# Kernel tuning notes

Measured on AMD Instinct MI355X. Metric: run time of the kernel, lower is better.

## Reference

```python
import jax, jax.numpy as jnp
import numpy as np

B, N, C = 2, 4096, 1024
H, WIN = 16, 20
D = C // H

def setup_inputs() -> dict:
    key = jax.random.key(0)
    ks = jax.random.split(key, 9)
    s = 1.0 / np.sqrt(C)
    d = {"q": jax.random.normal(ks[0], (B, N, C), jnp.float32)}
    for i, name in enumerate(["Wq", "Wk", "Wv", "Wo"]):
        d[name + "_w"] = jax.random.normal(ks[1 + 2 * i], (C, C), jnp.float32) * s
        d[name + "_b"] = jax.random.normal(ks[2 + 2 * i], (C,), jnp.float32) * 0.01
    return d

def reference(q, Wq_w, Wq_b, Wk_w, Wk_b, Wv_w, Wv_b, Wo_w, Wo_b):
    b, n, c = q.shape
    w2 = WIN // 2  # half window = 10
    def proj(x, w, bias):
        return (x @ w.T + bias).reshape(b, n, H, D).transpose(0, 2, 1, 3)  # [B,H,N,D]
    Q = proj(q, Wq_w, Wq_b)
    K = proj(q, Wk_w, Wk_b)
    V = proj(q, Wv_w, Wv_b)
    off = jnp.arange(-w2, w2 + 1)                       # [Wn] = 21 offsets
    pos = jnp.arange(n)[:, None] + off[None, :]         # [N, Wn] key index per query
    valid = (pos >= 0) & (pos < n)                      # edge clipping == torch start/end slicing
    idx = jnp.clip(pos, 0, n - 1)
    Kw = K[:, :, idx, :]                                # [B,H,N,Wn,D] gathered key windows
    Vw = V[:, :, idx, :]
    scale = jnp.sqrt(jnp.float32(D))
    scores = jnp.einsum('bhnd,bhnwd->bhnw', Q, Kw) / scale
    scores = jnp.where(valid[None, None], scores, -jnp.inf)
    probs = jax.nn.softmax(scores, axis=-1)             # invalid slots get exactly 0
    out = jnp.einsum('bhnw,bhnwd->bhnd', probs, Vw)
    out = out.transpose(0, 2, 1, 3).reshape(b, n, c)
    out = out @ Wo_w.T + Wo_b
    # torch returns attn_probs of the LAST loop iteration i=N-1: window [N-1-w2, N), size w2+1
    attn_last = probs[:, :, -1:, : w2 + 1]              # [B,H,1,11]
    return (out, attn_last)
```

## Files before the change

kernel.cpp:

```cpp
#include <hip/hip_runtime.h>
#include <hip/hip_bf16.h>

#define Bb 2
#define Nn 4096
#define Cc 1024
#define Hh 16
#define Dd 64
#define Mm (Bb*Nn)
#define W2 10
#define WINSZ 21

typedef __attribute__((ext_vector_type(8))) short  bf16x8s;
typedef __attribute__((ext_vector_type(4))) float  f32x4;
typedef __attribute__((ext_vector_type(4))) unsigned short us4;

#define AS1 __attribute__((address_space(1)))
#define AS3 __attribute__((address_space(3)))

__device__ __forceinline__ unsigned short f2bf(float f) {
  unsigned int u = __float_as_uint(f);
  u += 0x7FFFu + ((u >> 16) & 1u);
  return (unsigned short)(u >> 16);
}
__device__ __forceinline__ float bflo(unsigned int u) { return __uint_as_float(u << 16); }
__device__ __forceinline__ float bfhi(unsigned int u) { return __uint_as_float(u & 0xFFFF0000u); }

__global__ __launch_bounds__(256) void f2bf_kernel(const float4* __restrict__ src,
                                                   us4* __restrict__ dst, int n4) {
  int stride = gridDim.x * 256;
  for (int i = blockIdx.x * 256 + threadIdx.x; i < n4; i += stride) {
    float4 v = src[i];
    us4 o;
    o.x = f2bf(v.x); o.y = f2bf(v.y); o.z = f2bf(v.z); o.w = f2bf(v.w);
    dst[i] = o;
  }
}

template<bool OUT_BF16>
__global__ __launch_bounds__(512) void gemm_p3(const unsigned short* __restrict__ A,
                                               const unsigned short* __restrict__ Bm,
                                               const float* __restrict__ bias,
                                               void* __restrict__ Cout,
                                               int N) {
  constexpr int K = 1024, NT = 16;
  __shared__ unsigned short lds[3][24576];

  const int tid = threadIdx.x, wid = tid >> 6, lane = tid & 63;
  const int wm = wid >> 2, wn = wid & 3;

  const int nwg = gridDim.x, cpx = nwg >> 3, bid = blockIdx.x;
  const int swz = (bid & 7) * cpx + (bid >> 3);
  const int nbn = N >> 8;
  const int m0 = (swz / nbn) << 7, n0 = (swz % nbn) << 8;

  const int rbase = wid * 8 + (lane >> 3);
  const int cst = ((lane & 7) ^ (lane >> 3)) * 8;
  const unsigned short* aS0 = A + (size_t)(m0 + rbase) * K + cst;
  const unsigned short* aS1 = A + (size_t)(m0 + 64 + rbase) * K + cst;
  const unsigned short* bS0 = Bm + (size_t)(n0 + rbase) * K + cst;
  const unsigned short* bS1 = Bm + (size_t)(n0 + 64 + rbase) * K + cst;
  const unsigned short* bS2 = Bm + (size_t)(n0 + 128 + rbase) * K + cst;
  const unsigned short* bS3 = Bm + (size_t)(n0 + 192 + rbase) * K + cst;
  const int dA0 = wid * 512, dA1 = 4096 + wid * 512;
  const int dB0 = 8192 + wid * 512, dB1 = 12288 + wid * 512;
  const int dB2 = 16384 + wid * 512, dB3 = 20480 + wid * 512;

#define STG(bf, kt) do {                                                                   \
    const size_t ko = (size_t)(kt) * 64;                                                   \
    __builtin_amdgcn_global_load_lds((AS1 const void*)(aS0 + ko), (AS3 void*)(&lds[bf][dA0]), 16, 0, 0); \
    __builtin_amdgcn_global_load_lds((AS1 const void*)(aS1 + ko), (AS3 void*)(&lds[bf][dA1]), 16, 0, 0); \
    __builtin_amdgcn_global_load_lds((AS1 const void*)(bS0 + ko), (AS3 void*)(&lds[bf][dB0]), 16, 0, 0); \
    __builtin_amdgcn_global_load_lds((AS1 const void*)(bS1 + ko), (AS3 void*)(&lds[bf][dB1]), 16, 0, 0); \
    __builtin_amdgcn_global_load_lds((AS1 const void*)(bS2 + ko), (AS3 void*)(&lds[bf][dB2]), 16, 0, 0); \
    __builtin_amdgcn_global_load_lds((AS1 const void*)(bS3 + ko), (AS3 void*)(&lds[bf][dB3]), 16, 0, 0); \
  } while (0)

  int aoff[2][4], boff[2][4];
#pragma unroll
  for (int kk = 0; kk < 2; ++kk) {
    const int chs = ((kk * 4 + (lane >> 4)) ^ (lane & 7)) * 8;
#pragma unroll
    for (int f = 0; f < 4; ++f) {
      aoff[kk][f] = (wm * 64 + f * 16 + (lane & 15)) * 64 + chs;
      boff[kk][f] = 8192 + (wn * 64 + f * 16 + (lane & 15)) * 64 + chs;
    }
  }

  f32x4 acc[4][4] = {};

  STG(0, 0);
  STG(1, 1);
  asm volatile("s_waitcnt vmcnt(6)" ::: "memory");
  __builtin_amdgcn_sched_barrier(0);
  __builtin_amdgcn_s_barrier();
  __builtin_amdgcn_sched_barrier(0);

  int cur = 0, stg = 2;
  for (int t = 0; t < NT; ++t) {
    if (t + 2 < NT) STG(stg, t + 2);

    const unsigned short* L = &lds[cur][0];
    bf16x8s a[2][4], b[2][4];
#pragma unroll
    for (int kk = 0; kk < 2; ++kk) {
#pragma unroll
      for (int f = 0; f < 4; ++f) {
        a[kk][f] = *(const bf16x8s*)(L + aoff[kk][f]);
        b[kk][f] = *(const bf16x8s*)(L + boff[kk][f]);
      }
    }
    __builtin_amdgcn_s_setprio(1);
#pragma unroll
    for (int kk = 0; kk < 2; ++kk)
#pragma unroll
      for (int fm = 0; fm < 4; ++fm)
#pragma unroll
        for (int fn = 0; fn < 4; ++fn)
          acc[fm][fn] = __builtin_amdgcn_mfma_f32_16x16x32_bf16(a[kk][fm], b[kk][fn], acc[fm][fn], 0, 0, 0);
    __builtin_amdgcn_s_setprio(0);

    if (t + 1 < NT) {
      if (t + 2 < NT) asm volatile("s_waitcnt vmcnt(6)" ::: "memory");
      else            asm volatile("s_waitcnt vmcnt(0)" ::: "memory");
      __builtin_amdgcn_sched_barrier(0);
      __builtin_amdgcn_s_barrier();
      __builtin_amdgcn_sched_barrier(0);
    }
    cur = (cur == 2) ? 0 : cur + 1;
    stg = (stg == 2) ? 0 : stg + 1;
  }
#undef STG

  const int r0 = m0 + wm * 64 + (lane >> 4) * 4;
  const int c0 = n0 + wn * 64 + (lane & 15);
#pragma unroll
  for (int fm = 0; fm < 4; ++fm) {
#pragma unroll
    for (int fn = 0; fn < 4; ++fn) {
      const int col = c0 + fn * 16;
      const float bv = bias[col];
#pragma unroll
      for (int r = 0; r < 4; ++r) {
        const int row = r0 + fm * 16 + r;
        const float v = acc[fm][fn][r] + bv;
        if (OUT_BF16)
          ((unsigned short*)Cout)[(size_t)row * N + col] = f2bf(v);
        else
          ((float*)Cout)[(size_t)row * N + col] = v;
      }
    }
  }
}

#define TN 128
#define KVROWS (TN + 2 * W2)

__global__ void attn_kernel(const unsigned short* __restrict__ QKV,
                            unsigned short* __restrict__ AO,
                            float* __restrict__ attn_last) {
  __shared__ uint4 Kl[KVROWS * 8];
  __shared__ uint4 Vl[KVROWS * 8];

  const int nt = Nn / TN;
  const int bid = blockIdx.x;
  const int tile = bid & (nt - 1);
  const int bh = bid / nt;
  const int h = bh & (Hh - 1), b = bh / Hh;
  const int n0 = tile * TN;
  const int tid = threadIdx.x;

  for (int idx = tid; idx < KVROWS * 8; idx += 256) {
    const int r = idx >> 3, c = idx & 7;
    const int pos = n0 - W2 + r;
    uint4 kv = make_uint4(0, 0, 0, 0), vv = make_uint4(0, 0, 0, 0);
    if (pos >= 0 && pos < Nn) {
      const uint4* row = (const uint4*)(QKV + (size_t)(b * Nn + pos) * 3072);
      kv = row[128 + h * 8 + c];
      vv = row[256 + h * 8 + c];
    }
    const int slot = c ^ (r & 7);
    Kl[r * 8 + slot] = kv;
    Vl[r * 8 + slot] = vv;
  }
  __syncthreads();

  const int row  = tid >> 1;
  const int half = tid & 1;
  const int n = n0 + row;
  const size_t m = (size_t)b * Nn + n;

  const uint4* qrow = (const uint4*)(QKV + m * 3072) + h * 8 + half * 4;
  const uint4 qd0 = qrow[0], qd1 = qrow[1], qd2 = qrow[2], qd3 = qrow[3];

  float p[WINSZ];
#pragma unroll
  for (int w = 0; w < WINSZ; ++w) p[w] = 0.f;

#pragma unroll
  for (int c = 0; c < 4; ++c) {
    const uint4 qv = (c == 0) ? qd0 : (c == 1) ? qd1 : (c == 2) ? qd2 : qd3;
    const float q0 = bflo(qv.x), q1 = bfhi(qv.x);
    const float q2 = bflo(qv.y), q3 = bfhi(qv.y);
    const float q4 = bflo(qv.z), q5 = bfhi(qv.z);
    const float q6 = bflo(qv.w), q7 = bfhi(qv.w);
#pragma unroll 7
    for (int w = 0; w < WINSZ; ++w) {
      const int r = row + w;
      const uint4 v = Kl[r * 8 + ((half * 4 + c) ^ (r & 7))];
      float a0 = q0 * bflo(v.x);
      float a1 = q1 * bfhi(v.x);
      a0 += q2 * bflo(v.y);
      a1 += q3 * bfhi(v.y);
      a0 += q4 * bflo(v.z);
      a1 += q5 * bfhi(v.z);
      a0 += q6 * bflo(v.w);
      a1 += q7 * bfhi(v.w);
      p[w] += a0 + a1;
    }
  }

#pragma unroll
  for (int w = 0; w < WINSZ; ++w) {
    float t = p[w];
    t += __shfl_xor(t, 1, 64);
    const int pos = n - W2 + w;
    p[w] = (pos < 0 || pos >= Nn) ? -1e30f : t * 0.125f;
  }
  float mx = p[0];
#pragma unroll
  for (int w = 1; w < WINSZ; ++w) mx = fmaxf(mx, p[w]);
  float sum = 0.f;
#pragma unroll
  for (int w = 0; w < WINSZ; ++w) { p[w] = __expf(p[w] - mx); sum += p[w]; }
  const float inv = 1.0f / sum;

  if (n == Nn - 1 && half == 0) {
#pragma unroll
    for (int w = 0; w <= W2; ++w)
      attn_last[(b * Hh + h) * (W2 + 1) + w] = p[w] * inv;
  }

  uint4* orow = (uint4*)(AO + m * Cc + h * Dd) + half * 4;
#pragma unroll
  for (int c = 0; c < 4; ++c) {
    float o0 = 0.f, o1 = 0.f, o2 = 0.f, o3 = 0.f;
    float o4 = 0.f, o5 = 0.f, o6 = 0.f, o7 = 0.f;
#pragma unroll 7
    for (int w = 0; w < WINSZ; ++w) {
      const int r = row + w;
      const uint4 v = Vl[r * 8 + ((half * 4 + c) ^ (r & 7))];
      const float pw = p[w];
      o0 += pw * bflo(v.x);
      o1 += pw * bfhi(v.x);
      o2 += pw * bflo(v.y);
      o3 += pw * bfhi(v.y);
      o4 += pw * bflo(v.z);
      o5 += pw * bfhi(v.z);
      o6 += pw * bflo(v.w);
      o7 += pw * bfhi(v.w);
    }
    unsigned int d0 = (unsigned int)f2bf(o0 * inv) | ((unsigned int)f2bf(o1 * inv) << 16);
    unsigned int d1 = (unsigned int)f2bf(o2 * inv) | ((unsigned int)f2bf(o3 * inv) << 16);
    unsigned int d2 = (unsigned int)f2bf(o4 * inv) | ((unsigned int)f2bf(o5 * inv) << 16);
    unsigned int d3 = (unsigned int)f2bf(o6 * inv) | ((unsigned int)f2bf(o7 * inv) << 16);
    orow[c] = make_uint4(d0, d1, d2, d3);
  }
}

extern "C" void kernel_launch(void* const* d_in, const int* in_sizes, int n_in,
                              void* d_out, int out_size, void* d_ws, size_t ws_size,
                              hipStream_t stream) {
  const float* q    = (const float*)d_in[0];
  const float* Wq_w = (const float*)d_in[1];
  const float* Wq_b = (const float*)d_in[2];
  const float* Wk_w = (const float*)d_in[3];
  const float* Wk_b = (const float*)d_in[4];
  const float* Wv_w = (const float*)d_in[5];
  const float* Wv_b = (const float*)d_in[6];
  const float* Wo_w = (const float*)d_in[7];
  const float* Wo_b = (const float*)d_in[8];
  float* out = (float*)d_out;
  float* attn_last = out + (size_t)Mm * Cc;

  char* ws = (char*)d_ws;
  unsigned short* qb   = (unsigned short*)(ws);
  unsigned short* Wqkv = (unsigned short*)(ws + 16777216);
  unsigned short* Wo16 = (unsigned short*)(ws + 16777216 + 6291456);
  float*          bqkv = (float*)(ws + 25165824);
  unsigned short* QKV  = (unsigned short*)(ws + 25182208);
  unsigned short* AO   = (unsigned short*)(ws + 75513856);

  {
    int n4 = (Mm * Cc) / 4;
    f2bf_kernel<<<2048, 256, 0, stream>>>((const float4*)q, (us4*)qb, n4);
    int w4 = (Cc * Cc) / 4;
    f2bf_kernel<<<1024, 256, 0, stream>>>((const float4*)Wq_w, (us4*)(Wqkv), w4);
    f2bf_kernel<<<1024, 256, 0, stream>>>((const float4*)Wk_w, (us4*)(Wqkv + Cc * Cc), w4);
    f2bf_kernel<<<1024, 256, 0, stream>>>((const float4*)Wv_w, (us4*)(Wqkv + 2 * Cc * Cc), w4);
    f2bf_kernel<<<1024, 256, 0, stream>>>((const float4*)Wo_w, (us4*)Wo16, w4);
    hipMemcpyAsync(bqkv,          Wq_b, Cc * sizeof(float), hipMemcpyDeviceToDevice, stream);
    hipMemcpyAsync(bqkv + Cc,     Wk_b, Cc * sizeof(float), hipMemcpyDeviceToDevice, stream);
    hipMemcpyAsync(bqkv + 2 * Cc, Wv_b, Cc * sizeof(float), hipMemcpyDeviceToDevice, stream);
  }

  {
    dim3 grid((Mm / 128) * (3072 / 256));
    gemm_p3<true><<<grid, 512, 0, stream>>>(qb, Wqkv, bqkv, (void*)QKV, 3072);
  }

  {
    dim3 grid(Bb * Hh * (Nn / TN));
    attn_kernel<<<grid, 256, 0, stream>>>(QKV, AO, attn_last);
  }

  {
    dim3 grid((Mm / 128) * (Cc / 256));
    gemm_p3<false><<<grid, 512, 0, stream>>>(AO, Wo16, Wo_b, (void*)out, Cc);
  }
}
```

Measured before the change: 150.7 us.

## Enlarge GEMM tiles to 256x256 with double-buffered LDS staging

The bf16 MFMA GEMM block tile grows from 128x256 to 256x256, with each wave computing 128x64 outputs and 8x4 accumulator fragments. The LDS pipeline moves from triple to double buffering with a full vmcnt(0) wait each iteration. The aim is more reuse per global load and fewer workgroups. In exchange, register pressure rises, LDS use reaches 128KB so only one workgroup fits per CU, and the output GEMM's grid falls below the CU count.

```diff
diff --git a/kernel.cpp b/kernel.cpp
--- a/kernel.cpp
+++ b/kernel.cpp
@@ -37,13 +37,13 @@
 }
 
 template<bool OUT_BF16>
-__global__ __launch_bounds__(512) void gemm_p3(const unsigned short* __restrict__ A,
+__global__ __launch_bounds__(512) void gemm256(const unsigned short* __restrict__ A,
                                                const unsigned short* __restrict__ Bm,
                                                const float* __restrict__ bias,
                                                void* __restrict__ Cout,
                                                int N) {
   constexpr int K = 1024, NT = 16;
-  __shared__ unsigned short lds[3][24576];
+  __shared__ unsigned short lds[2][32768];
 
   const int tid = threadIdx.x, wid = tid >> 6, lane = tid & 63;
   const int wm = wid >> 2, wn = wid & 3;
@@ -51,90 +51,86 @@
   const int nwg = gridDim.x, cpx = nwg >> 3, bid = blockIdx.x;
   const int swz = (bid & 7) * cpx + (bid >> 3);
   const int nbn = N >> 8;
-  const int m0 = (swz / nbn) << 7, n0 = (swz % nbn) << 8;
+  const int m0 = (swz / nbn) << 8, n0 = (swz % nbn) << 8;
 
   const int rbase = wid * 8 + (lane >> 3);
   const int cst = ((lane & 7) ^ (lane >> 3)) * 8;
-  const unsigned short* aS0 = A + (size_t)(m0 + rbase) * K + cst;
-  const unsigned short* aS1 = A + (size_t)(m0 + 64 + rbase) * K + cst;
-  const unsigned short* bS0 = Bm + (size_t)(n0 + rbase) * K + cst;
-  const unsigned short* bS1 = Bm + (size_t)(n0 + 64 + rbase) * K + cst;
-  const unsigned short* bS2 = Bm + (size_t)(n0 + 128 + rbase) * K + cst;
-  const unsigned short* bS3 = Bm + (size_t)(n0 + 192 + rbase) * K + cst;
-  const int dA0 = wid * 512, dA1 = 4096 + wid * 512;
-  const int dB0 = 8192 + wid * 512, dB1 = 12288 + wid * 512;
-  const int dB2 = 16384 + wid * 512, dB3 = 20480 + wid * 512;
-
-#define STG(bf, kt) do {                                                                   \
-    const size_t ko = (size_t)(kt) * 64;                                                   \
-    __builtin_amdgcn_global_load_lds((AS1 const void*)(aS0 + ko), (AS3 void*)(&lds[bf][dA0]), 16, 0, 0); \
-    __builtin_amdgcn_global_load_lds((AS1 const void*)(aS1 + ko), (AS3 void*)(&lds[bf][dA1]), 16, 0, 0); \
-    __builtin_amdgcn_global_load_lds((AS1 const void*)(bS0 + ko), (AS3 void*)(&lds[bf][dB0]), 16, 0, 0); \
-    __builtin_amdgcn_global_load_lds((AS1 const void*)(bS1 + ko), (AS3 void*)(&lds[bf][dB1]), 16, 0, 0); \
-    __builtin_amdgcn_global_load_lds((AS1 const void*)(bS2 + ko), (AS3 void*)(&lds[bf][dB2]), 16, 0, 0); \
-    __builtin_amdgcn_global_load_lds((AS1 const void*)(bS3 + ko), (AS3 void*)(&lds[bf][dB3]), 16, 0, 0); \
+  const unsigned short* aS[4];
+  const unsigned short* bS[4];
+#pragma unroll
+  for (int q = 0; q < 4; ++q) {
+    aS[q] = A  + (size_t)(m0 + q * 64 + rbase) * K + cst;
+    bS[q] = Bm + (size_t)(n0 + q * 64 + rbase) * K + cst;
+  }
+  const int dst0 = wid * 512;
+
+#define STG(bf, kt) do {                                                                     \
+    const size_t ko = (size_t)(kt) * 64;                                                     \
+    __builtin_amdgcn_global_load_lds((AS1 const void*)(aS[0] + ko), (AS3 void*)(&lds[bf][        dst0]), 16, 0, 0); \
+    __builtin_amdgcn_global_load_lds((AS1 const void*)(aS[1] + ko), (AS3 void*)(&lds[bf][ 4096 + dst0]), 16, 0, 0); \
+    __builtin_amdgcn_global_load_lds((AS1 const void*)(aS[2] + ko), (AS3 void*)(&lds[bf][ 8192 + dst0]), 16, 0, 0); \
+    __builtin_amdgcn_global_load_lds((AS1 const void*)(aS[3] + ko), (AS3 void*)(&lds[bf][12288 + dst0]), 16, 0, 0); \
+    __builtin_amdgcn_global_load_lds((AS1 const void*)(bS[0] + ko), (AS3 void*)(&lds[bf][16384 + dst0]), 16, 0, 0); \
+    __builtin_amdgcn_global_load_lds((AS1 const void*)(bS[1] + ko), (AS3 void*)(&lds[bf][20480 + dst0]), 16, 0, 0); \
+    __builtin_amdgcn_global_load_lds((AS1 const void*)(bS[2] + ko), (AS3 void*)(&lds[bf][24576 + dst0]), 16, 0, 0); \
+    __builtin_amdgcn_global_load_lds((AS1 const void*)(bS[3] + ko), (AS3 void*)(&lds[bf][28672 + dst0]), 16, 0, 0); \
   } while (0)
 
-  int aoff[2][4], boff[2][4];
+  int aoff[2][8], boff[2][4];
 #pragma unroll
   for (int kk = 0; kk < 2; ++kk) {
     const int chs = ((kk * 4 + (lane >> 4)) ^ (lane & 7)) * 8;
 #pragma unroll
-    for (int f = 0; f < 4; ++f) {
-      aoff[kk][f] = (wm * 64 + f * 16 + (lane & 15)) * 64 + chs;
-      boff[kk][f] = 8192 + (wn * 64 + f * 16 + (lane & 15)) * 64 + chs;
-    }
-  }
-
-  f32x4 acc[4][4] = {};
+    for (int f = 0; f < 8; ++f)
+      aoff[kk][f] = (wm * 128 + f * 16 + (lane & 15)) * 64 + chs;
+#pragma unroll
+    for (int f = 0; f < 4; ++f)
+      boff[kk][f] = 16384 + (wn * 64 + f * 16 + (lane & 15)) * 64 + chs;
+  }
+
+  f32x4 acc[8][4] = {};
 
   STG(0, 0);
-  STG(1, 1);
-  asm volatile("s_waitcnt vmcnt(6)" ::: "memory");
+  asm volatile("s_waitcnt vmcnt(0)" ::: "memory");
   __builtin_amdgcn_sched_barrier(0);
   __builtin_amdgcn_s_barrier();
   __builtin_amdgcn_sched_barrier(0);
 
-  int cur = 0, stg = 2;
+  int cur = 0;
   for (int t = 0; t < NT; ++t) {
-    if (t + 2 < NT) STG(stg, t + 2);
+    if (t + 1 < NT) STG(cur ^ 1, t + 1);
 
     const unsigned short* L = &lds[cur][0];
-    bf16x8s a[2][4], b[2][4];
 #pragma unroll
     for (int kk = 0; kk < 2; ++kk) {
-#pragma unroll
-      for (int f = 0; f < 4; ++f) {
-        a[kk][f] = *(const bf16x8s*)(L + aoff[kk][f]);
-        b[kk][f] = *(const bf16x8s*)(L + boff[kk][f]);
-      }
-    }
-    __builtin_amdgcn_s_setprio(1);
-#pragma unroll
-    for (int kk = 0; kk < 2; ++kk)
-#pragma unroll
-      for (int fm = 0; fm < 4; ++fm)
+      bf16x8s a[8], b[4];
+#pragma unroll
+      for (int f = 0; f < 8; ++f) a[f] = *(const bf16x8s*)(L + aoff[kk][f]);
+#pragma unroll
+      for (int f = 0; f < 4; ++f) b[f] = *(const bf16x8s*)(L + boff[kk][f]);
+      __builtin_amdgcn_s_setprio(1);
+#pragma unroll
+      for (int fm = 0; fm < 8; ++fm)
 #pragma unroll
         for (int fn = 0; fn < 4; ++fn)
-          acc[fm][fn] = __builtin_amdgcn_mfma_f32_16x16x32_bf16(a[kk][fm], b[kk][fn], acc[fm][fn], 0, 0, 0);
-    __builtin_amdgcn_s_setprio(0);
+          acc[fm][fn] = __builtin_amdgcn_mfma_f32_16x16x32_bf16(a[fm], b[fn], acc[fm][fn], 0, 0, 0);
+      __builtin_amdgcn_s_setprio(0);
+    }
 
     if (t + 1 < NT) {
-      if (t + 2 < NT) asm volatile("s_waitcnt vmcnt(6)" ::: "memory");
-      else            asm volatile("s_waitcnt vmcnt(0)" ::: "memory");
+      asm volatile("s_waitcnt vmcnt(0)" ::: "memory");
       __builtin_amdgcn_sched_barrier(0);
       __builtin_amdgcn_s_barrier();
       __builtin_amdgcn_sched_barrier(0);
     }
-    cur = (cur == 2) ? 0 : cur + 1;
-    stg = (stg == 2) ? 0 : stg + 1;
+    cur ^= 1;
   }
 #undef STG
 
-  const int r0 = m0 + wm * 64 + (lane >> 4) * 4;
+  const int r0 = m0 + wm * 128 + (lane >> 4) * 4;
   const int c0 = n0 + wn * 64 + (lane & 15);
 #pragma unroll
-  for (int fm = 0; fm < 4; ++fm) {
+  for (int fm = 0; fm < 8; ++fm) {
 #pragma unroll
     for (int fn = 0; fn < 4; ++fn) {
       const int col = c0 + fn * 16;
@@ -304,8 +300,8 @@
   }
 
   {
-    dim3 grid((Mm / 128) * (3072 / 256));
-    gemm_p3<true><<<grid, 512, 0, stream>>>(qb, Wqkv, bqkv, (void*)QKV, 3072);
+    dim3 grid((Mm / 256) * (3072 / 256));
+    gemm256<true><<<grid, 512, 0, stream>>>(qb, Wqkv, bqkv, (void*)QKV, 3072);
   }
 
   {
@@ -314,7 +310,7 @@
   }
 
   {
-    dim3 grid((Mm / 128) * (Cc / 256));
-    gemm_p3<false><<<grid, 512, 0, stream>>>(AO, Wo16, Wo_b, (void*)out, Cc);
-  }
-}
+    dim3 grid((Mm / 256) * (Cc / 256));
+    gemm256<false><<<grid, 512, 0, stream>>>(AO, Wo16, Wo_b, (void*)out, Cc);
+  }
+}
```

After: 152.8 us. No clear change (+1.4%).

## Fuse conversion kernels and bias copies into one launch; swap GEMM tile order

Applied to the files above, without the earlier changes.

Replaces five separate fp32-to-bf16 conversion launches and three device-to-device bias memcpys with a single grid-stride kernel that converts the input and all four weights and copies the biases. This removes seven launch and memcpy overheads and the gaps between them. It also changes the GEMM tile mapping so the M-tile index varies fastest within the swizzled order instead of the N-tile, which changes which A/B tiles are reused in cache across neighbouring workgroups.

```diff
diff --git a/kernel.cpp b/kernel.cpp
--- a/kernel.cpp
+++ b/kernel.cpp
@@ -25,14 +25,42 @@
 __device__ __forceinline__ float bflo(unsigned int u) { return __uint_as_float(u << 16); }
 __device__ __forceinline__ float bfhi(unsigned int u) { return __uint_as_float(u & 0xFFFF0000u); }
 
-__global__ __launch_bounds__(256) void f2bf_kernel(const float4* __restrict__ src,
-                                                   us4* __restrict__ dst, int n4) {
-  int stride = gridDim.x * 256;
-  for (int i = blockIdx.x * 256 + threadIdx.x; i < n4; i += stride) {
-    float4 v = src[i];
-    us4 o;
-    o.x = f2bf(v.x); o.y = f2bf(v.y); o.z = f2bf(v.z); o.w = f2bf(v.w);
-    dst[i] = o;
+__device__ __forceinline__ us4 cvt4(float4 v) {
+  us4 o;
+  o.x = f2bf(v.x); o.y = f2bf(v.y); o.z = f2bf(v.z); o.w = f2bf(v.w);
+  return o;
+}
+
+__global__ __launch_bounds__(256) void cvt_all(const float4* __restrict__ q,
+                                               const float4* __restrict__ wq,
+                                               const float4* __restrict__ wk,
+                                               const float4* __restrict__ wv,
+                                               const float4* __restrict__ wo,
+                                               const float* __restrict__ bq,
+                                               const float* __restrict__ bk,
+                                               const float* __restrict__ bv,
+                                               us4* __restrict__ qb4,
+                                               us4* __restrict__ wqkv4,
+                                               us4* __restrict__ wo4,
+                                               float* __restrict__ bqkv) {
+  const int NQ = 2097152, NW = 262144, TOT = NQ + 4 * NW;
+  const int gid = blockIdx.x * 256 + threadIdx.x;
+  const int stride = gridDim.x * 256;
+  for (int i = gid; i < TOT; i += stride) {
+    if (i < NQ) {
+      qb4[i] = cvt4(q[i]);
+    } else {
+      int j = i - NQ;
+      int r = j >> 18, k = j & (NW - 1);
+      if (r == 0)      wqkv4[k]          = cvt4(wq[k]);
+      else if (r == 1) wqkv4[NW + k]     = cvt4(wk[k]);
+      else if (r == 2) wqkv4[2 * NW + k] = cvt4(wv[k]);
+      else             wo4[k]            = cvt4(wo[k]);
+    }
+  }
+  if (gid < 3072) {
+    float v = (gid < 1024) ? bq[gid] : (gid < 2048) ? bk[gid - 1024] : bv[gid - 2048];
+    bqkv[gid] = v;
   }
 }
 
@@ -42,7 +70,7 @@
                                                const float* __restrict__ bias,
                                                void* __restrict__ Cout,
                                                int N) {
-  constexpr int K = 1024, NT = 16;
+  constexpr int K = 1024, NT = 16, NBM = Mm / 128;
   __shared__ unsigned short lds[3][24576];
 
   const int tid = threadIdx.x, wid = tid >> 6, lane = tid & 63;
@@ -50,8 +78,7 @@
 
   const int nwg = gridDim.x, cpx = nwg >> 3, bid = blockIdx.x;
   const int swz = (bid & 7) * cpx + (bid >> 3);
-  const int nbn = N >> 8;
-  const int m0 = (swz / nbn) << 7, n0 = (swz % nbn) << 8;
+  const int m0 = (swz % NBM) << 7, n0 = (swz / NBM) << 8;
 
   const int rbase = wid * 8 + (lane >> 3);
   const int cst = ((lane & 7) ^ (lane >> 3)) * 8;
@@ -290,18 +317,11 @@
   unsigned short* QKV  = (unsigned short*)(ws + 25182208);
   unsigned short* AO   = (unsigned short*)(ws + 75513856);
 
-  {
-    int n4 = (Mm * Cc) / 4;
-    f2bf_kernel<<<2048, 256, 0, stream>>>((const float4*)q, (us4*)qb, n4);
-    int w4 = (Cc * Cc) / 4;
-    f2bf_kernel<<<1024, 256, 0, stream>>>((const float4*)Wq_w, (us4*)(Wqkv), w4);
-    f2bf_kernel<<<1024, 256, 0, stream>>>((const float4*)Wk_w, (us4*)(Wqkv + Cc * Cc), w4);
-    f2bf_kernel<<<1024, 256, 0, stream>>>((const float4*)Wv_w, (us4*)(Wqkv + 2 * Cc * Cc), w4);
-    f2bf_kernel<<<1024, 256, 0, stream>>>((const float4*)Wo_w, (us4*)Wo16, w4);
-    hipMemcpyAsync(bqkv,          Wq_b, Cc * sizeof(float), hipMemcpyDeviceToDevice, stream);
-    hipMemcpyAsync(bqkv + Cc,     Wk_b, Cc * sizeof(float), hipMemcpyDeviceToDevice, stream);
-    hipMemcpyAsync(bqkv + 2 * Cc, Wv_b, Cc * sizeof(float), hipMemcpyDeviceToDevice, stream);
-  }
+  cvt_all<<<2048, 256, 0, stream>>>((const float4*)q,
+                                    (const float4*)Wq_w, (const float4*)Wk_w,
+                                    (const float4*)Wv_w, (const float4*)Wo_w,
+                                    Wq_b, Wk_b, Wv_b,
+                                    (us4*)qb, (us4*)Wqkv, (us4*)Wo16, bqkv);
 
   {
     dim3 grid((Mm / 128) * (3072 / 256));
```

Result: faster. 134.5 us (-10.7%).
